# Kernel optimization log

Hardware: AMD Instinct MI355X
Metric: run time of the kernel (lower is better)

The kernel has to match this reference:

```python
import jax, jax.numpy as jnp
import numpy as np

N_SRC, N_DST, E = 100000, 10000, 320000
F_IN, HID, NCLS = 128, 256, 3
NEG_SLOPE = 0.2


def setup_inputs() -> dict:
    key = jax.random.key(0)
    ks = jax.random.split(key, 10)
    return {
        "x_src": jax.random.normal(ks[0], (N_SRC, F_IN), jnp.float32),
        "x_dst": jax.random.normal(ks[1], (N_DST, F_IN), jnp.float32),
        "edge_src": jax.random.randint(ks[2], (E,), 0, N_SRC),
        "edge_dst": jax.random.randint(ks[3], (E,), 0, N_DST),
        "W": jax.random.normal(ks[4], (F_IN, HID), jnp.float32) * (1.0 / np.sqrt(F_IN)),
        "att_src": jax.random.normal(ks[5], (HID,), jnp.float32) * 0.1,
        "att_dst": jax.random.normal(ks[6], (HID,), jnp.float32) * 0.1,
        "bias": jnp.zeros((HID,), jnp.float32),
        "Wc": jax.random.normal(ks[7], (HID, NCLS), jnp.float32) * (1.0 / np.sqrt(HID)),
        "bc": jnp.zeros((NCLS,), jnp.float32),
    }


def reference(x_src, x_dst, edge_src, edge_dst, W, att_src, att_dst, bias, Wc, bc):
    # Linear transform (heads=1, out=256)
    h_src = x_src @ W                      # [N_src, H]
    h_dst = x_dst @ W                      # [N_dst, H]
    # Per-node attention contributions, then gather per edge
    a_src = h_src @ att_src                # [N_src]
    a_dst = h_dst @ att_dst                # [N_dst]
    logits = jax.nn.leaky_relu(a_dst[edge_dst] + a_src[edge_src], NEG_SLOPE)  # [E]
    # Segment softmax over incoming edges of each destination node
    m = jax.ops.segment_max(logits, edge_dst, num_segments=N_DST)
    e = jnp.exp(logits - m[edge_dst])
    denom = jax.ops.segment_sum(e, edge_dst, num_segments=N_DST) + 1e-16
    alpha = e / denom[edge_dst]            # [E]
    # Weighted scatter-sum of source messages
    out = jax.ops.segment_sum(alpha[:, None] * h_src[edge_src], edge_dst, num_segments=N_DST)
    out = out + bias                       # [N_dst, H]
    scores = out @ Wc + bc                 # [N_dst, 3]
    return jax.nn.log_softmax(scores, axis=1)
```

## Files before the change

### kernel.cpp

```cpp
#include <hip/hip_runtime.h>
#include <float.h>

#define NSRC 100000
#define NDST 10000
#define NEDGE 320000
#define FIN 128
#define HID 256
#define NCLS 3
#define NEG_SLOPE 0.2f

#define RANGES 4
#define REPL 128
#define DPB (NDST / RANGES)
#define EPB (NEDGE / REPL)
#define TPB 1024

__global__ void prep_kernel(const float* __restrict__ W, const float* __restrict__ att_src,
                            const float* __restrict__ att_dst, const float* __restrict__ bias,
                            const float* __restrict__ Wc, const float* __restrict__ bc,
                            float* __restrict__ wa_src, float* __restrict__ wa_dst,
                            float* __restrict__ wfc, float* __restrict__ bf) {
  int l = threadIdx.x;
  if (blockIdx.x < FIN) {
    int k = blockIdx.x;
    float4 w = ((const float4*)(W + (size_t)k * HID))[l];
    int h0 = 4 * l;
    float s1 = w.x * att_src[h0] + w.y * att_src[h0 + 1] + w.z * att_src[h0 + 2] + w.w * att_src[h0 + 3];
    float s2 = w.x * att_dst[h0] + w.y * att_dst[h0 + 1] + w.z * att_dst[h0 + 2] + w.w * att_dst[h0 + 3];
    float f0 = w.x * Wc[h0 * NCLS] + w.y * Wc[(h0 + 1) * NCLS] + w.z * Wc[(h0 + 2) * NCLS] + w.w * Wc[(h0 + 3) * NCLS];
    float f1 = w.x * Wc[h0 * NCLS + 1] + w.y * Wc[(h0 + 1) * NCLS + 1] + w.z * Wc[(h0 + 2) * NCLS + 1] + w.w * Wc[(h0 + 3) * NCLS + 1];
    float f2 = w.x * Wc[h0 * NCLS + 2] + w.y * Wc[(h0 + 1) * NCLS + 2] + w.z * Wc[(h0 + 2) * NCLS + 2] + w.w * Wc[(h0 + 3) * NCLS + 2];
#pragma unroll
    for (int off = 32; off; off >>= 1) {
      s1 += __shfl_down(s1, off);
      s2 += __shfl_down(s2, off);
      f0 += __shfl_down(f0, off);
      f1 += __shfl_down(f1, off);
      f2 += __shfl_down(f2, off);
    }
    if (l == 0) {
      wa_src[k] = s1;
      wa_dst[k] = s2;
      wfc[0 * FIN + k] = f0;
      wfc[1 * FIN + k] = f1;
      wfc[2 * FIN + k] = f2;
    }
  } else {
    float b0 = 0.f, b1 = 0.f, b2 = 0.f;
#pragma unroll
    for (int j = 0; j < 4; ++j) {
      int h = l + 64 * j;
      float bi = bias[h];
      b0 += bi * Wc[h * NCLS + 0];
      b1 += bi * Wc[h * NCLS + 1];
      b2 += bi * Wc[h * NCLS + 2];
    }
#pragma unroll
    for (int off = 32; off; off >>= 1) {
      b0 += __shfl_down(b0, off);
      b1 += __shfl_down(b1, off);
      b2 += __shfl_down(b2, off);
    }
    if (l == 0) {
      bf[0] = b0 + bc[0];
      bf[1] = b1 + bc[1];
      bf[2] = b2 + bc[2];
    }
  }
}

__global__ void matvec_fused_kernel(const float* __restrict__ x_src, const float* __restrict__ x_dst,
                                    const float* __restrict__ wa_src, const float* __restrict__ wa_dst,
                                    const float* __restrict__ wfc, float* __restrict__ a_src,
                                    float* __restrict__ a_dst, float4* __restrict__ q4) {
  int gid = blockIdx.x * blockDim.x + threadIdx.x;
  int row = gid >> 5;
  int l = threadIdx.x & 31;
  if (row < NSRC) {
    float4 v = ((const float4*)(x_src + (size_t)row * FIN))[l];
    float4 w = ((const float4*)wa_src)[l];
    float4 c0 = ((const float4*)(wfc + 0 * FIN))[l];
    float4 c1 = ((const float4*)(wfc + 1 * FIN))[l];
    float4 c2 = ((const float4*)(wfc + 2 * FIN))[l];
    float p0 = v.x * w.x + v.y * w.y + v.z * w.z + v.w * w.w;
    float p1 = v.x * c0.x + v.y * c0.y + v.z * c0.z + v.w * c0.w;
    float p2 = v.x * c1.x + v.y * c1.y + v.z * c1.z + v.w * c1.w;
    float p3 = v.x * c2.x + v.y * c2.y + v.z * c2.z + v.w * c2.w;
#pragma unroll
    for (int off = 16; off; off >>= 1) {
      p0 += __shfl_down(p0, off);
      p1 += __shfl_down(p1, off);
      p2 += __shfl_down(p2, off);
      p3 += __shfl_down(p3, off);
    }
    if (l == 0) {
      a_src[row] = p0;
      q4[row] = make_float4(p1, p2, p3, 1.0f);
    }
  } else {
    int rd = row - NSRC;
    if (rd >= NDST) return;
    float4 v = ((const float4*)(x_dst + (size_t)rd * FIN))[l];
    float4 w = ((const float4*)wa_dst)[l];
    float p = v.x * w.x + v.y * w.y + v.z * w.z + v.w * w.w;
#pragma unroll
    for (int off = 16; off; off >>= 1) p += __shfl_down(p, off);
    if (l == 0) a_dst[rd] = p;
  }
}

__global__ __launch_bounds__(TPB) void edge_lds_kernel(
    const int* __restrict__ edge_src, const int* __restrict__ edge_dst,
    const float* __restrict__ a_src, const float* __restrict__ a_dst,
    const float4* __restrict__ q4, float* __restrict__ partial) {
  __shared__ float lacc[DPB * 4];
  int c = blockIdx.x;
  int r = blockIdx.y;
  int tid = threadIdx.x;
  for (int i = tid; i < DPB * 4; i += TPB) lacc[i] = 0.f;
  __syncthreads();

  int d0 = r * DPB;
  int ebase = c * EPB;
  for (int i = tid; i < EPB; i += TPB) {
    int e = ebase + i;
    int d = edge_dst[e];
    unsigned dr = (unsigned)(d - d0);
    if (dr < (unsigned)DPB) {
      int s = edge_src[e];
      float z = a_dst[d] + a_src[s];
      float logit = (z >= 0.f) ? z : NEG_SLOPE * z;
      float w = __expf(logit);
      float4 qv = q4[s];
      float* b = lacc + dr * 4;
      atomicAdd(b + 0, w * qv.x);
      atomicAdd(b + 1, w * qv.y);
      atomicAdd(b + 2, w * qv.z);
      atomicAdd(b + 3, w);
    }
  }
  __syncthreads();

  float* dst = partial + ((size_t)r * REPL + c) * (DPB * 4);
  for (int i = tid; i < DPB * 4; i += TPB) dst[i] = lacc[i];
}

__global__ void merge_finalize_kernel(const float4* __restrict__ partial,
                                      const float* __restrict__ bf, float* __restrict__ out) {
  int d = blockIdx.x * blockDim.x + threadIdx.x;
  if (d >= NDST) return;
  int r = d / DPB;
  int dr = d - r * DPB;
  const float4* base = partial + (size_t)r * REPL * DPB + dr;
  float a0 = 0.f, a1 = 0.f, a2 = 0.f, aw = 0.f;
#pragma unroll 8
  for (int c = 0; c < REPL; ++c) {
    float4 v = base[(size_t)c * DPB];
    a0 += v.x;
    a1 += v.y;
    a2 += v.z;
    aw += v.w;
  }
  float inv = 1.f / (aw + 1e-16f);
  float s0 = a0 * inv + bf[0];
  float s1 = a1 * inv + bf[1];
  float s2 = a2 * inv + bf[2];
  float mx = fmaxf(s0, fmaxf(s1, s2));
  float l = logf(__expf(s0 - mx) + __expf(s1 - mx) + __expf(s2 - mx));
  out[d * NCLS + 0] = s0 - mx - l;
  out[d * NCLS + 1] = s1 - mx - l;
  out[d * NCLS + 2] = s2 - mx - l;
}

extern "C" void kernel_launch(void* const* d_in, const int* in_sizes, int n_in,
                              void* d_out, int out_size, void* d_ws, size_t ws_size,
                              hipStream_t stream) {
  const float* x_src    = (const float*)d_in[0];
  const float* x_dst    = (const float*)d_in[1];
  const int*   edge_src = (const int*)d_in[2];
  const int*   edge_dst = (const int*)d_in[3];
  const float* W        = (const float*)d_in[4];
  const float* att_src  = (const float*)d_in[5];
  const float* att_dst  = (const float*)d_in[6];
  const float* bias     = (const float*)d_in[7];
  const float* Wc       = (const float*)d_in[8];
  const float* bc       = (const float*)d_in[9];
  float* out = (float*)d_out;

  char* p = (char*)d_ws;
  auto carve = [&](size_t bytes) {
    void* r = (void*)p;
    p += (bytes + 255) & ~(size_t)255;
    return r;
  };
  float*  wa_src  = (float*)carve(FIN * 4);
  float*  wa_dst  = (float*)carve(FIN * 4);
  float*  wfc     = (float*)carve(NCLS * FIN * 4);
  float*  bf      = (float*)carve(NCLS * 4);
  float*  a_src   = (float*)carve((size_t)NSRC * 4);
  float*  a_dst   = (float*)carve((size_t)NDST * 4);
  float4* q4      = (float4*)carve((size_t)NSRC * 16);
  float*  partial = (float*)carve((size_t)RANGES * REPL * DPB * 4 * 4);

  prep_kernel<<<FIN + 1, 64, 0, stream>>>(W, att_src, att_dst, bias, Wc, bc,
                                          wa_src, wa_dst, wfc, bf);
  {
    int rows = NSRC + NDST;
    int blocks = (rows * 32 + 255) / 256;
    matvec_fused_kernel<<<blocks, 256, 0, stream>>>(x_src, x_dst, wa_src, wa_dst, wfc,
                                                    a_src, a_dst, q4);
  }
  edge_lds_kernel<<<dim3(REPL, RANGES), TPB, 0, stream>>>(edge_src, edge_dst, a_src, a_dst,
                                                          q4, partial);
  merge_finalize_kernel<<<(NDST + 255) / 256, 256, 0, stream>>>((const float4*)partial, bf, out);
}
```

Before: 127.8 us.

## Pack a_src into q4, stage a_dst in LDS, halve edge replicas

The per-source attention scalar now goes into the fourth lane of the q4 float4, replacing the constant 1. This removes the separate a_src array and one random gather per edge. Each edge block copies its range's a_dst slice into shared memory, writes partials as float4, and the replica count drops from 128 to 64. The goal is fewer scattered global loads and less partial-buffer traffic for the merge kernel. The cost is fewer edge blocks (256 instead of 512), which lowers parallelism and raises LDS atomic contention per block.

```diff
diff --git a/kernel.cpp b/kernel.cpp
--- a/kernel.cpp
+++ b/kernel.cpp
@@ -10,7 +10,7 @@
 #define NEG_SLOPE 0.2f
 
 #define RANGES 4
-#define REPL 128
+#define REPL 64
 #define DPB (NDST / RANGES)
 #define EPB (NEDGE / REPL)
 #define TPB 1024
@@ -71,8 +71,8 @@
 
 __global__ void matvec_fused_kernel(const float* __restrict__ x_src, const float* __restrict__ x_dst,
                                     const float* __restrict__ wa_src, const float* __restrict__ wa_dst,
-                                    const float* __restrict__ wfc, float* __restrict__ a_src,
-                                    float* __restrict__ a_dst, float4* __restrict__ q4) {
+                                    const float* __restrict__ wfc, float* __restrict__ a_dst,
+                                    float4* __restrict__ q4) {
   int gid = blockIdx.x * blockDim.x + threadIdx.x;
   int row = gid >> 5;
   int l = threadIdx.x & 31;
@@ -93,10 +93,7 @@
       p2 += __shfl_down(p2, off);
       p3 += __shfl_down(p3, off);
     }
-    if (l == 0) {
-      a_src[row] = p0;
-      q4[row] = make_float4(p1, p2, p3, 1.0f);
-    }
+    if (l == 0) q4[row] = make_float4(p1, p2, p3, p0);
   } else {
     int rd = row - NSRC;
     if (rd >= NDST) return;
@@ -111,16 +108,18 @@
 
 __global__ __launch_bounds__(TPB) void edge_lds_kernel(
     const int* __restrict__ edge_src, const int* __restrict__ edge_dst,
-    const float* __restrict__ a_src, const float* __restrict__ a_dst,
-    const float4* __restrict__ q4, float* __restrict__ partial) {
+    const float* __restrict__ a_dst, const float4* __restrict__ q4,
+    float4* __restrict__ partial) {
   __shared__ float lacc[DPB * 4];
+  __shared__ float ladst[DPB];
   int c = blockIdx.x;
   int r = blockIdx.y;
   int tid = threadIdx.x;
+  int d0 = r * DPB;
   for (int i = tid; i < DPB * 4; i += TPB) lacc[i] = 0.f;
+  for (int i = tid; i < DPB; i += TPB) ladst[i] = a_dst[d0 + i];
   __syncthreads();
 
-  int d0 = r * DPB;
   int ebase = c * EPB;
   for (int i = tid; i < EPB; i += TPB) {
     int e = ebase + i;
@@ -128,21 +127,22 @@
     unsigned dr = (unsigned)(d - d0);
     if (dr < (unsigned)DPB) {
       int s = edge_src[e];
-      float z = a_dst[d] + a_src[s];
+      float4 qv = q4[s];
+      float z = ladst[dr] + qv.w;
       float logit = (z >= 0.f) ? z : NEG_SLOPE * z;
       float w = __expf(logit);
-      float4 qv = q4[s];
-      float* b = lacc + dr * 4;
-      atomicAdd(b + 0, w * qv.x);
-      atomicAdd(b + 1, w * qv.y);
-      atomicAdd(b + 2, w * qv.z);
-      atomicAdd(b + 3, w);
+      float* bp = lacc + dr * 4;
+      atomicAdd(bp + 0, w * qv.x);
+      atomicAdd(bp + 1, w * qv.y);
+      atomicAdd(bp + 2, w * qv.z);
+      atomicAdd(bp + 3, w);
     }
   }
   __syncthreads();
 
-  float* dst = partial + ((size_t)r * REPL + c) * (DPB * 4);
-  for (int i = tid; i < DPB * 4; i += TPB) dst[i] = lacc[i];
+  float4* dst = partial + ((size_t)r * REPL + c) * DPB;
+  float4* lv = (float4*)lacc;
+  for (int i = tid; i < DPB; i += TPB) dst[i] = lv[i];
 }
 
 __global__ void merge_finalize_kernel(const float4* __restrict__ partial,
@@ -151,7 +151,7 @@
   if (d >= NDST) return;
   int r = d / DPB;
   int dr = d - r * DPB;
-  const float4* base = partial + (size_t)r * REPL * DPB + dr;
+  const float4* base = partial + (size_t)(r * REPL) * DPB + dr;
   float a0 = 0.f, a1 = 0.f, a2 = 0.f, aw = 0.f;
 #pragma unroll 8
   for (int c = 0; c < REPL; ++c) {
@@ -197,10 +197,9 @@
   float*  wa_dst  = (float*)carve(FIN * 4);
   float*  wfc     = (float*)carve(NCLS * FIN * 4);
   float*  bf      = (float*)carve(NCLS * 4);
-  float*  a_src   = (float*)carve((size_t)NSRC * 4);
   float*  a_dst   = (float*)carve((size_t)NDST * 4);
   float4* q4      = (float4*)carve((size_t)NSRC * 16);
-  float*  partial = (float*)carve((size_t)RANGES * REPL * DPB * 4 * 4);
+  float4* partial = (float4*)carve((size_t)RANGES * REPL * DPB * 16);
 
   prep_kernel<<<FIN + 1, 64, 0, stream>>>(W, att_src, att_dst, bias, Wc, bc,
                                           wa_src, wa_dst, wfc, bf);
@@ -208,9 +207,8 @@
     int rows = NSRC + NDST;
     int blocks = (rows * 32 + 255) / 256;
     matvec_fused_kernel<<<blocks, 256, 0, stream>>>(x_src, x_dst, wa_src, wa_dst, wfc,
-                                                    a_src, a_dst, q4);
-  }
-  edge_lds_kernel<<<dim3(REPL, RANGES), TPB, 0, stream>>>(edge_src, edge_dst, a_src, a_dst,
-                                                          q4, partial);
-  merge_finalize_kernel<<<(NDST + 255) / 256, 256, 0, stream>>>((const float4*)partial, bf, out);
-}
+                                                    a_dst, q4);
+  }
+  edge_lds_kernel<<<dim3(REPL, RANGES), TPB, 0, stream>>>(edge_src, edge_dst, a_dst, q4, partial);
+  merge_finalize_kernel<<<(NDST + 255) / 256, 256, 0, stream>>>(partial, bf, out);
+}
```

Result: no change. 126.0 us (-1.4%).
